# Kernel tuning notes

Hardware: AMD Instinct MI355X
Metric: run time of the kernel (lower is better)

Reference implementation:

```python
import math
import jax, jax.numpy as jnp
import numpy as np

HEAD_DIM = 64
N_HEAD = 8
INIT_SIZE = 1200  # -> 1201 embeddings, origin_shift = 601


def rel_sinusoidal_pos_embed(seq_len, dim=HEAD_DIM):
    """Matches RelativeSinusoidalPositionalEmbedding(dim, padding_idx=0, init_size=1200)."""
    num = INIT_SIZE + 1  # 1201
    half = dim // 2
    inv_freq = jnp.exp(jnp.arange(half, dtype=jnp.float32) * -(math.log(10000.0) / (half - 1)))
    pos = jnp.arange(-(num // 2), num // 2, dtype=jnp.float32)  # -601 .. 599 (1201 values)
    ang = pos[:, None] * inv_freq[None, :]                      # [num, half]
    w = jnp.concatenate([jnp.sin(ang), jnp.cos(ang)], axis=1)   # [num, dim]
    w = w.at[0].set(0.0)  # padding_idx row zeroed
    origin_shift = num // 2 + 1  # 601
    idx = jnp.arange(-seq_len, seq_len) + origin_shift          # [2L]
    return w[idx]                                               # [2L, dim]


def _shift(BD):
    # BD: [b, n, L, 2L] -> [b, n, L, L] (Transformer-XL skew trick)
    b, n, L, _ = BD.shape
    BD = jnp.pad(BD, ((0, 0), (0, 0), (0, 0), (0, 1)))  # [b,n,L,2L+1]
    BD = BD.reshape(b, n, 2 * L + 1, L)[:, :, :-1].reshape(b, n, L, 2 * L)
    return BD[:, :, :, L:]


def _transpose_shift(E):
    # E: [b, n, L, 2L] -> [b, n, L, L]
    b, n, L, _ = E.shape
    E = jnp.pad(E, ((0, 0), (0, 0), (0, 0), (0, 1))).reshape(b, n, 2 * L + 1, L)
    idx = jnp.arange(L) * 2 + 1
    return jnp.swapaxes(E[:, :, idx, :], -1, -2)


def setup_inputs() -> dict:
    key = jax.random.key(0)
    k1, k2, k3, k4 = jax.random.split(key, 4)
    B, L, D = 8, 512, 512
    x = jax.random.normal(k1, (B, L, D), dtype=jnp.float32)
    mask = jnp.ones((B, L), dtype=jnp.int32)
    W_qkv = jax.random.normal(k2, (D, 3 * D), dtype=jnp.float32) * (1.0 / math.sqrt(D))
    r_r_bias = jax.random.normal(k3, (N_HEAD, HEAD_DIM), dtype=jnp.float32) * 0.1
    r_w_bias = jax.random.normal(k4, (N_HEAD, HEAD_DIM), dtype=jnp.float32) * 0.1
    return {"x": x, "mask": mask, "W_qkv": W_qkv, "r_r_bias": r_r_bias, "r_w_bias": r_w_bias}


def reference(x, mask, W_qkv, r_r_bias, r_w_bias):
    B, L, D = x.shape
    scale = math.sqrt(HEAD_DIM)
    pos = rel_sinusoidal_pos_embed(L)  # [2L, head_dim], detached constant

    qkv = x @ W_qkv  # [B, L, 3D]
    q, k, v = jnp.split(qkv, 3, axis=-1)
    q = q.reshape(B, L, N_HEAD, HEAD_DIM).transpose(0, 2, 1, 3)  # [B,H,L,d]
    k = k.reshape(B, L, N_HEAD, HEAD_DIM).transpose(0, 2, 1, 3)
    v = v.reshape(B, L, N_HEAD, HEAD_DIM).transpose(0, 2, 1, 3)

    rw_head_q = q + r_r_bias[None, :, None, :]
    AC = jnp.einsum('bnqd,bnkd->bnqk', rw_head_q, k)              # [B,H,L,L]
    D_ = jnp.einsum('nd,ld->nl', r_w_bias, pos)[None, :, None, :] # [1,H,1,2L]
    B_ = jnp.einsum('bnqd,ld->bnql', q, pos)                      # [B,H,L,2L]
    E_ = jnp.einsum('bnqd,ld->bnql', k, pos)                      # [B,H,L,2L]

    BDE = _shift(B_ + D_) + _transpose_shift(E_)                  # [B,H,L,L]
    attn = (AC + BDE) / scale
    attn = jnp.where(mask[:, None, None, :] == 0, -jnp.inf, attn)
    attn = jax.nn.softmax(attn, axis=-1)

    out = jnp.matmul(attn, v)                                     # [B,H,L,d]
    return out.transpose(0, 2, 1, 3).reshape(B, L, D)
```

## Files before the change

kernel.cpp:

```cpp
#include <hip/hip_runtime.h>
#include <hip/hip_bf16.h>
#include <math.h>

#define LSEQ 512
#define DDIM 192

typedef __attribute__((ext_vector_type(8))) short s16x8;
typedef __attribute__((ext_vector_type(4))) float f32x4;
typedef unsigned short ushort_t;
typedef unsigned int uint_t;

#define MFMA16(a, b, c) __builtin_amdgcn_mfma_f32_16x16x32_bf16(a, b, c, 0, 0, 0)

__device__ __forceinline__ ushort_t f2b(float f) {
  union { float f; uint_t u; } v; v.f = f;
  uint_t r = (v.u + 0x7FFFu + ((v.u >> 16) & 1u)) >> 16;
  return (ushort_t)r;
}
__device__ __forceinline__ float b2f(ushort_t u) {
  union { uint_t u; float f; } v; v.u = ((uint_t)u) << 16;
  return v.f;
}

typedef const __attribute__((address_space(1))) void g_void_t;
typedef __attribute__((address_space(3))) void lds_void_t;
__device__ __forceinline__ void load_lds16(const void* g, void* l) {
  __builtin_amdgcn_global_load_lds((g_void_t*)g, (lds_void_t*)l, 16, 0, 0);
}

__device__ __forceinline__ size_t kswz(size_t row, int d) {
  return row * DDIM + (size_t)((d & 0x1C7) | ((((d >> 3) & 7) ^ ((int)row & 7)) << 3));
}

__global__ void cast_x(const float* __restrict__ x, ushort_t* __restrict__ xb) {
  const int i = (blockIdx.x * 256 + threadIdx.x) * 8;
  const int row = i >> 9, k = i & 511;
  float4 a = *(const float4*)(x + i);
  float4 b = *(const float4*)(x + i + 4);
  uint4 o;
  o.x = (uint_t)f2b(a.x) | ((uint_t)f2b(a.y) << 16);
  o.y = (uint_t)f2b(a.z) | ((uint_t)f2b(a.w) << 16);
  o.z = (uint_t)f2b(b.x) | ((uint_t)f2b(b.y) << 16);
  o.w = (uint_t)f2b(b.z) | ((uint_t)f2b(b.w) << 16);
  const int dst = row * 512 + (k & 448) + (((((k >> 3) & 7) ^ (row & 7))) << 3);
  *(uint4*)(xb + dst) = o;
}

__global__ void cast_transpose_w(const float* __restrict__ W, ushort_t* __restrict__ Wt) {
  __shared__ float tile[32][33];
  const int tx = threadIdx.x & 31, ty = threadIdx.x >> 5;
  const int k0 = blockIdx.x * 32, n0 = blockIdx.y * 32;
#pragma unroll
  for (int i = 0; i < 4; ++i)
    tile[ty + i * 8][tx] = W[(size_t)(k0 + ty + i * 8) * 1536 + n0 + tx];
  __syncthreads();
#pragma unroll
  for (int i = 0; i < 4; ++i) {
    const int n = n0 + ty + i * 8, k = k0 + tx;
    Wt[(size_t)n * 512 + (k & 448) + ((((k >> 3) & 7) ^ (n & 7)) << 3) + (k & 7)] =
        f2b(tile[tx][ty + i * 8]);
  }
}

__global__ __launch_bounds__(256, 3) void qkv_gemm(
    const ushort_t* __restrict__ xb, const ushort_t* __restrict__ Wt,
    const float* __restrict__ rr,
    ushort_t* __restrict__ Qt, ushort_t* __restrict__ Kt, ushort_t* __restrict__ Vt) {
  __shared__ __align__(16) ushort_t ldsA[2][64 * 64];
  __shared__ __align__(16) ushort_t ldsB[2][128 * 64];
  const int tid = threadIdx.x;
  const int w = tid >> 6, lane = tid & 63, lo = lane & 15, hi = lane >> 4;
  const int wm = w >> 1, wn = w & 1;
  const int id = blockIdx.x;
  const int mp = id & 63, np = id >> 6;
  const int m0 = mp * 64, n0 = np * 128;

  f32x4 acc[2][4];
  const f32x4 zero4 = {0.f, 0.f, 0.f, 0.f};
#pragma unroll
  for (int i = 0; i < 2; ++i)
#pragma unroll
    for (int j = 0; j < 4; ++j) acc[i][j] = zero4;

  const char* asrc = (const char*)xb + (size_t)m0 * 1024;
  const char* bsrc = (const char*)Wt + (size_t)n0 * 1024;

#define STAGE_QKV(buf, ks)                                                     \
  {                                                                            \
    char* la = (char*)&ldsA[buf][0] + w * 1024;                                \
    char* lb = (char*)&ldsB[buf][0] + w * 1024;                                \
    _Pragma("unroll") for (int it = 0; it < 2; ++it) {                         \
      const int X = it * 4096 + tid * 16;                                      \
      load_lds16(asrc + (size_t)(X >> 7) * 1024 + (ks) * 128 + (X & 127),      \
                 la + it * 4096);                                              \
    }                                                                          \
    _Pragma("unroll") for (int it = 0; it < 4; ++it) {                         \
      const int X = it * 4096 + tid * 16;                                      \
      load_lds16(bsrc + (size_t)(X >> 7) * 1024 + (ks) * 128 + (X & 127),      \
                 lb + it * 4096);                                              \
    }                                                                          \
  }

  STAGE_QKV(0, 0);
  for (int ks = 0; ks < 8; ++ks) {
    const int cur = ks & 1;
    __syncthreads();
    if (ks < 7) STAGE_QKV(cur ^ 1, ks + 1);
    const char* Ab = (const char*)&ldsA[cur][0];
    const char* Bb = (const char*)&ldsB[cur][0];
#pragma unroll
    for (int kh = 0; kh < 2; ++kh) {
      const int sw = ((kh * 4 + hi) ^ (lo & 7)) << 4;
      s16x8 a[2], bf[4];
#pragma unroll
      for (int i = 0; i < 2; ++i)
        a[i] = *(const s16x8*)(Ab + (wm * 32 + i * 16 + lo) * 128 + sw);
#pragma unroll
      for (int j = 0; j < 4; ++j)
        bf[j] = *(const s16x8*)(Bb + (wn * 64 + j * 16 + lo) * 128 + sw);
#pragma unroll
      for (int i = 0; i < 2; ++i)
#pragma unroll
        for (int j = 0; j < 4; ++j)
          acc[i][j] = MFMA16(a[i], bf[j], acc[i][j]);
    }
  }

  const int sect = n0 >> 9;
  const int h = ((n0 + wn * 64) >> 6) & 7;
  const int mrow0 = m0 + wm * 32;

  if (sect == 0) {
    float bias[4];
#pragma unroll
    for (int j = 0; j < 4; ++j) bias[j] = rr[h * 64 + j * 16 + lo];
#pragma unroll
    for (int i = 0; i < 2; ++i)
#pragma unroll
      for (int r = 0; r < 4; ++r) {
        const int m = mrow0 + i * 16 + hi * 4 + r;
        const size_t row = ((size_t)(m >> 9) * 8 + h) * 512 + (m & 511);
#pragma unroll
        for (int j = 0; j < 4; ++j)
          Qt[row * DDIM + j * 16 + lo] = f2b((acc[i][j][r] + bias[j]) * 0.125f);
      }
  } else if (sect == 1) {
#pragma unroll
    for (int i = 0; i < 2; ++i)
#pragma unroll
      for (int r = 0; r < 4; ++r) {
        const int m = mrow0 + i * 16 + hi * 4 + r;
        const size_t row = ((size_t)(m >> 9) * 8 + h) * 512 + (m & 511);
#pragma unroll
        for (int j = 0; j < 4; ++j)
          Kt[row * DDIM + ((((j * 2 + (lo >> 3)) ^ (m & 7)) << 3) | (lo & 7))] =
              f2b(acc[i][j][r]);
      }
  } else {
#pragma unroll
    for (int i = 0; i < 2; ++i) {
      const int b = (mrow0 + i * 16) >> 9;
      const int l0 = (mrow0 + i * 16 + hi * 4) & 511;
#pragma unroll
      for (int j = 0; j < 4; ++j) {
        ushort4 pk;
        pk.x = f2b(acc[i][j][0]); pk.y = f2b(acc[i][j][1]);
        pk.z = f2b(acc[i][j][2]); pk.w = f2b(acc[i][j][3]);
        *(ushort4*)&Vt[(((size_t)b * 8 + h) * 64 + j * 16 + lo) * 512 + l0] = pk;
      }
    }
  }
}

__global__ void build_feats(ushort_t* __restrict__ Qt, ushort_t* __restrict__ Kt,
                            const float* __restrict__ rr, const float* __restrict__ rw) {
  const int idx = blockIdx.x * blockDim.x + threadIdx.x;
  const int hf = idx & 31;
  const size_t row = (size_t)(idx >> 5);
  const int l = (int)(row & 511);
  const int hh = (int)((row >> 9) & 7);

  const float f = __expf(-(float)hf * 0.29710775393472f);
  float s0, c0, s1, c1;
  __sincosf((float)l * f, &s0, &c0);
  __sincosf((float)(l + 1) * f, &s1, &c1);

  const size_t qb = row * DDIM;
  const float qr_s = b2f(Qt[qb + hf]);
  const float qr_c = b2f(Qt[qb + 32 + hf]);
  const float qw_s = qr_s + 0.125f * (rw[hh * 64 + hf] - rr[hh * 64 + hf]);
  const float qw_c = qr_c + 0.125f * (rw[hh * 64 + 32 + hf] - rr[hh * 64 + 32 + hf]);
  Qt[qb + 64 + hf]  = f2b(qw_s * c0 + qw_c * s0);
  Qt[qb + 96 + hf]  = f2b(qw_c * c0 - qw_s * s0);
  Qt[qb + 128 + hf] = f2b(0.125f * s1);
  Qt[qb + 160 + hf] = f2b(0.125f * c1);

  const float k_s = b2f(Kt[kswz(row, hf)]);
  const float k_c = b2f(Kt[kswz(row, 32 + hf)]);
  Kt[kswz(row, 64 + hf)]  = f2b(s1);
  Kt[kswz(row, 96 + hf)]  = f2b(c1);
  Kt[kswz(row, 128 + hf)] = f2b(k_s * c0 + k_c * s0);
  Kt[kswz(row, 160 + hf)] = f2b(k_c * c0 - k_s * s0);
}

__global__ __launch_bounds__(256, 2) void attn_kernel(
    const ushort_t* __restrict__ Qt, const ushort_t* __restrict__ Kt,
    const ushort_t* __restrict__ Vt, const int* __restrict__ mask,
    float* __restrict__ out) {
  __shared__ __align__(16) ushort_t ldsK[2][64 * DDIM];
  __shared__ __align__(16) ushort_t P[4][16][72];

  const int tid = threadIdx.x;
  const int w = tid >> 6;
  const int lane = tid & 63, lo = lane & 15, hi = lane >> 4;
  const int id = blockIdx.x;
  const int bh = id & 63, qg = id >> 6;
  const int b = bh >> 3, h = bh & 7;
  const int q0 = qg * 64 + w * 16;
  const size_t qrow0 = (size_t)bh * LSEQ + q0;

  s16x8 qf[6];
#pragma unroll
  for (int ks = 0; ks < 6; ++ks)
    qf[ks] = *(const s16x8*)(Qt + (qrow0 + lo) * DDIM + ks * 32 + hi * 8);

  const f32x4 zero4 = {0.f, 0.f, 0.f, 0.f};
  f32x4 o[4];
#pragma unroll
  for (int j = 0; j < 4; ++j) o[j] = zero4;
  float mrun = -3.0e38f, lrun = 0.f;

  const char* ksrc = (const char*)(Kt + (size_t)bh * LSEQ * DDIM);
  const ushort_t* vbase = Vt + ((size_t)bh * 64 + lo) * 512 + hi * 8;

  {
    char* d = (char*)&ldsK[0][0] + w * 1024;
#pragma unroll
    for (int it = 0; it < 6; ++it)
      load_lds16(ksrc + it * 4096 + tid * 16, d + it * 4096);
  }

  for (int kt = 0; kt < 8; ++kt) {
    const int cur = kt & 1;
    __syncthreads();
    if (kt < 7) {
      const char* s = ksrc + (kt + 1) * 24576;
      char* d = (char*)&ldsK[cur ^ 1][0] + w * 1024;
#pragma unroll
      for (int it = 0; it < 6; ++it)
        load_lds16(s + it * 4096 + tid * 16, d + it * 4096);
    }

    f32x4 sf[4];
#pragma unroll
    for (int f = 0; f < 4; ++f) sf[f] = zero4;
    const char* kl = (const char*)&ldsK[cur][0];
    __builtin_amdgcn_s_setprio(1);
#pragma unroll
    for (int ks = 0; ks < 6; ++ks) {
      const int swb = ((ks * 4 + hi) ^ (lo & 7)) << 4;
#pragma unroll
      for (int f = 0; f < 4; ++f) {
        s16x8 ka = *(const s16x8*)(kl + (f * 16 + lo) * 384 + swb);
        sf[f] = MFMA16(ka, qf[ks], sf[f]);
      }
    }
    __builtin_amdgcn_s_setprio(0);

    const int mk = mask[b * LSEQ + kt * 64 + lane];
    if (__ballot(mk == 0) != 0ull) {
#pragma unroll
      for (int f = 0; f < 4; ++f)
#pragma unroll
        for (int r = 0; r < 4; ++r)
          if (__shfl(mk, f * 16 + hi * 4 + r) == 0) sf[f][r] = -3.0e38f;
    }

    float tm = fmaxf(fmaxf(sf[0][0], sf[0][1]), fmaxf(sf[0][2], sf[0][3]));
#pragma unroll
    for (int f = 1; f < 4; ++f)
      tm = fmaxf(tm, fmaxf(fmaxf(sf[f][0], sf[f][1]), fmaxf(sf[f][2], sf[f][3])));
    tm = fmaxf(tm, __shfl_xor(tm, 16));
    tm = fmaxf(tm, __shfl_xor(tm, 32));

    if (!__all(tm - mrun <= 8.0f)) {
      const float mnew = fmaxf(mrun, tm);
      const float corr = __expf(mrun - mnew);
      lrun *= corr;
      mrun = mnew;
      float cq[4];
#pragma unroll
      for (int r = 0; r < 4; ++r) cq[r] = __shfl(corr, hi * 4 + r);
#pragma unroll
      for (int j = 0; j < 4; ++j)
#pragma unroll
        for (int r = 0; r < 4; ++r) o[j][r] *= cq[r];
    }

    float ts = 0.f;
#pragma unroll
    for (int f = 0; f < 4; ++f)
#pragma unroll
      for (int r = 0; r < 4; ++r) {
        sf[f][r] = __expf(sf[f][r] - mrun);
        ts += sf[f][r];
      }
    ts += __shfl_xor(ts, 16);
    ts += __shfl_xor(ts, 32);
    lrun += ts;

#pragma unroll
    for (int f = 0; f < 4; ++f) {
      __hip_bfloat162 p0 = __float22bfloat162_rn(make_float2(sf[f][0], sf[f][1]));
      __hip_bfloat162 p1 = __float22bfloat162_rn(make_float2(sf[f][2], sf[f][3]));
      uint2 u;
      __builtin_memcpy(&u.x, &p0, 4);
      __builtin_memcpy(&u.y, &p1, 4);
      *(uint2*)&P[w][lo][f * 16 + hi * 4] = u;
    }

    __builtin_amdgcn_s_setprio(1);
#pragma unroll
    for (int kh = 0; kh < 2; ++kh) {
      s16x8 pa = *(const s16x8*)&P[w][lo][kh * 32 + hi * 8];
#pragma unroll
      for (int j = 0; j < 4; ++j) {
        s16x8 vb = *(const s16x8*)(vbase + (size_t)j * 16 * 512 + kt * 64 + kh * 32);
        o[j] = MFMA16(pa, vb, o[j]);
      }
    }
    __builtin_amdgcn_s_setprio(0);
  }

  float lq[4];
#pragma unroll
  for (int r = 0; r < 4; ++r) lq[r] = 1.0f / __shfl(lrun, hi * 4 + r);
#pragma unroll
  for (int j = 0; j < 4; ++j)
#pragma unroll
    for (int r = 0; r < 4; ++r)
      out[((size_t)b * LSEQ + q0 + hi * 4 + r) * 512 + h * 64 + j * 16 + lo] =
          o[j][r] * lq[r];
}

extern "C" void kernel_launch(void* const* d_in, const int* in_sizes, int n_in,
                              void* d_out, int out_size, void* d_ws, size_t ws_size,
                              hipStream_t stream) {
  const float* x    = (const float*)d_in[0];
  const int*   mask = (const int*)d_in[1];
  const float* W    = (const float*)d_in[2];
  const float* rr   = (const float*)d_in[3];
  const float* rw   = (const float*)d_in[4];
  float* out = (float*)d_out;

  char* ws = (char*)d_ws;
  ushort_t* xb = (ushort_t*)(ws);
  ushort_t* Wt = (ushort_t*)(ws + 4194304);
  ushort_t* Qt = (ushort_t*)(ws + 5767168);
  ushort_t* Kt = (ushort_t*)(ws + 18350080);
  ushort_t* Vt = (ushort_t*)(ws + 30932992);

  cast_x<<<1024, 256, 0, stream>>>(x, xb);
  cast_transpose_w<<<dim3(16, 48), 256, 0, stream>>>(W, Wt);
  qkv_gemm<<<768, 256, 0, stream>>>(xb, Wt, rr, Qt, Kt, Vt);
  build_feats<<<4096, 256, 0, stream>>>(Qt, Kt, rr, rw);
  attn_kernel<<<512, 256, 0, stream>>>(Qt, Kt, Vt, mask, out);
}
```

Measured before the change: 60.75 us.

## Process 32 query rows per wave in attention and merge cast kernels

The attention kernel now uses 2 waves of 128 threads per block, each handling 32 query rows as two 16-row MFMA tiles. Each K fragment read from LDS and each V fragment loaded from global memory then feeds two MFMAs, which halves the fragment traffic per row. The two input-cast kernels are also merged into one launch to cut a kernel launch. In exchange, register pressure rises and there are fewer waves per block (launch bounds 128,1), which may reduce latency hiding and occupancy.

```diff
diff --git a/kernel.cpp b/kernel.cpp
--- a/kernel.cpp
+++ b/kernel.cpp
@@ -32,33 +32,36 @@
   return row * DDIM + (size_t)((d & 0x1C7) | ((((d >> 3) & 7) ^ ((int)row & 7)) << 3));
 }
 
-__global__ void cast_x(const float* __restrict__ x, ushort_t* __restrict__ xb) {
-  const int i = (blockIdx.x * 256 + threadIdx.x) * 8;
-  const int row = i >> 9, k = i & 511;
-  float4 a = *(const float4*)(x + i);
-  float4 b = *(const float4*)(x + i + 4);
-  uint4 o;
-  o.x = (uint_t)f2b(a.x) | ((uint_t)f2b(a.y) << 16);
-  o.y = (uint_t)f2b(a.z) | ((uint_t)f2b(a.w) << 16);
-  o.z = (uint_t)f2b(b.x) | ((uint_t)f2b(b.y) << 16);
-  o.w = (uint_t)f2b(b.z) | ((uint_t)f2b(b.w) << 16);
-  const int dst = row * 512 + (k & 448) + (((((k >> 3) & 7) ^ (row & 7))) << 3);
-  *(uint4*)(xb + dst) = o;
-}
-
-__global__ void cast_transpose_w(const float* __restrict__ W, ushort_t* __restrict__ Wt) {
+__global__ void cast_all(const float* __restrict__ x, const float* __restrict__ W,
+                         ushort_t* __restrict__ xb, ushort_t* __restrict__ Wt) {
   __shared__ float tile[32][33];
-  const int tx = threadIdx.x & 31, ty = threadIdx.x >> 5;
-  const int k0 = blockIdx.x * 32, n0 = blockIdx.y * 32;
-#pragma unroll
-  for (int i = 0; i < 4; ++i)
-    tile[ty + i * 8][tx] = W[(size_t)(k0 + ty + i * 8) * 1536 + n0 + tx];
-  __syncthreads();
-#pragma unroll
-  for (int i = 0; i < 4; ++i) {
-    const int n = n0 + ty + i * 8, k = k0 + tx;
-    Wt[(size_t)n * 512 + (k & 448) + ((((k >> 3) & 7) ^ (n & 7)) << 3) + (k & 7)] =
-        f2b(tile[tx][ty + i * 8]);
+  const int id = blockIdx.x;
+  if (id < 1024) {
+    const int i = (id * 256 + threadIdx.x) * 8;
+    const int row = i >> 9, k = i & 511;
+    float4 a = *(const float4*)(x + i);
+    float4 b = *(const float4*)(x + i + 4);
+    uint4 o;
+    o.x = (uint_t)f2b(a.x) | ((uint_t)f2b(a.y) << 16);
+    o.y = (uint_t)f2b(a.z) | ((uint_t)f2b(a.w) << 16);
+    o.z = (uint_t)f2b(b.x) | ((uint_t)f2b(b.y) << 16);
+    o.w = (uint_t)f2b(b.z) | ((uint_t)f2b(b.w) << 16);
+    const int dst = row * 512 + (k & 448) + (((((k >> 3) & 7) ^ (row & 7))) << 3);
+    *(uint4*)(xb + dst) = o;
+  } else {
+    const int wid = id - 1024;
+    const int tx = threadIdx.x & 31, ty = threadIdx.x >> 5;
+    const int k0 = (wid & 15) * 32, n0 = (wid >> 4) * 32;
+#pragma unroll
+    for (int i = 0; i < 4; ++i)
+      tile[ty + i * 8][tx] = W[(size_t)(k0 + ty + i * 8) * 1536 + n0 + tx];
+    __syncthreads();
+#pragma unroll
+    for (int i = 0; i < 4; ++i) {
+      const int n = n0 + ty + i * 8, k = k0 + tx;
+      Wt[(size_t)n * 512 + (k & 448) + ((((k >> 3) & 7) ^ (n & 7)) << 3) + (k & 7)] =
+          f2b(tile[tx][ty + i * 8]);
+    }
   }
 }
 
@@ -203,12 +206,12 @@
   Kt[kswz(row, 160 + hf)] = f2b(k_c * c0 - k_s * s0);
 }
 
-__global__ __launch_bounds__(256, 2) void attn_kernel(
+__global__ __launch_bounds__(128, 1) void attn_kernel(
     const ushort_t* __restrict__ Qt, const ushort_t* __restrict__ Kt,
     const ushort_t* __restrict__ Vt, const int* __restrict__ mask,
     float* __restrict__ out) {
   __shared__ __align__(16) ushort_t ldsK[2][64 * DDIM];
-  __shared__ __align__(16) ushort_t P[4][16][72];
+  __shared__ __align__(16) ushort_t P[2][32][72];
 
   const int tid = threadIdx.x;
   const int w = tid >> 6;
@@ -216,44 +219,47 @@
   const int id = blockIdx.x;
   const int bh = id & 63, qg = id >> 6;
   const int b = bh >> 3, h = bh & 7;
-  const int q0 = qg * 64 + w * 16;
+  const int q0 = qg * 64 + w * 32;
   const size_t qrow0 = (size_t)bh * LSEQ + q0;
 
-  s16x8 qf[6];
-#pragma unroll
-  for (int ks = 0; ks < 6; ++ks)
-    qf[ks] = *(const s16x8*)(Qt + (qrow0 + lo) * DDIM + ks * 32 + hi * 8);
+  s16x8 qf[2][6];
+#pragma unroll
+  for (int i = 0; i < 2; ++i)
+#pragma unroll
+    for (int ks = 0; ks < 6; ++ks)
+      qf[i][ks] = *(const s16x8*)(Qt + (qrow0 + i * 16 + lo) * DDIM + ks * 32 + hi * 8);
 
   const f32x4 zero4 = {0.f, 0.f, 0.f, 0.f};
-  f32x4 o[4];
-#pragma unroll
-  for (int j = 0; j < 4; ++j) o[j] = zero4;
-  float mrun = -3.0e38f, lrun = 0.f;
+  f32x4 o[2][4];
+#pragma unroll
+  for (int i = 0; i < 2; ++i)
+#pragma unroll
+    for (int j = 0; j < 4; ++j) o[i][j] = zero4;
+  float mrun[2] = {-3.0e38f, -3.0e38f}, lrun[2] = {0.f, 0.f};
 
   const char* ksrc = (const char*)(Kt + (size_t)bh * LSEQ * DDIM);
   const ushort_t* vbase = Vt + ((size_t)bh * 64 + lo) * 512 + hi * 8;
 
-  {
-    char* d = (char*)&ldsK[0][0] + w * 1024;
-#pragma unroll
-    for (int it = 0; it < 6; ++it)
-      load_lds16(ksrc + it * 4096 + tid * 16, d + it * 4096);
-  }
+#pragma unroll
+  for (int it = 0; it < 12; ++it)
+    load_lds16(ksrc + it * 2048 + tid * 16, (char*)&ldsK[0][0] + it * 2048 + tid * 16);
 
   for (int kt = 0; kt < 8; ++kt) {
     const int cur = kt & 1;
     __syncthreads();
     if (kt < 7) {
       const char* s = ksrc + (kt + 1) * 24576;
-      char* d = (char*)&ldsK[cur ^ 1][0] + w * 1024;
-#pragma unroll
-      for (int it = 0; it < 6; ++it)
-        load_lds16(s + it * 4096 + tid * 16, d + it * 4096);
-    }
-
-    f32x4 sf[4];
-#pragma unroll
-    for (int f = 0; f < 4; ++f) sf[f] = zero4;
+      char* d = (char*)&ldsK[cur ^ 1][0];
+#pragma unroll
+      for (int it = 0; it < 12; ++it)
+        load_lds16(s + it * 2048 + tid * 16, d + it * 2048 + tid * 16);
+    }
+
+    f32x4 sf[2][4];
+#pragma unroll
+    for (int i = 0; i < 2; ++i)
+#pragma unroll
+      for (int f = 0; f < 4; ++f) sf[i][f] = zero4;
     const char* kl = (const char*)&ldsK[cur][0];
     __builtin_amdgcn_s_setprio(1);
 #pragma unroll
@@ -262,7 +268,8 @@
 #pragma unroll
       for (int f = 0; f < 4; ++f) {
         s16x8 ka = *(const s16x8*)(kl + (f * 16 + lo) * 384 + swb);
-        sf[f] = MFMA16(ka, qf[ks], sf[f]);
+        sf[0][f] = MFMA16(ka, qf[0][ks], sf[0][f]);
+        sf[1][f] = MFMA16(ka, qf[1][ks], sf[1][f]);
       }
     }
     __builtin_amdgcn_s_setprio(0);
@@ -273,74 +280,86 @@
       for (int f = 0; f < 4; ++f)
 #pragma unroll
         for (int r = 0; r < 4; ++r)
-          if (__shfl(mk, f * 16 + hi * 4 + r) == 0) sf[f][r] = -3.0e38f;
-    }
-
-    float tm = fmaxf(fmaxf(sf[0][0], sf[0][1]), fmaxf(sf[0][2], sf[0][3]));
-#pragma unroll
-    for (int f = 1; f < 4; ++f)
-      tm = fmaxf(tm, fmaxf(fmaxf(sf[f][0], sf[f][1]), fmaxf(sf[f][2], sf[f][3])));
-    tm = fmaxf(tm, __shfl_xor(tm, 16));
-    tm = fmaxf(tm, __shfl_xor(tm, 32));
-
-    if (!__all(tm - mrun <= 8.0f)) {
-      const float mnew = fmaxf(mrun, tm);
-      const float corr = __expf(mrun - mnew);
-      lrun *= corr;
-      mrun = mnew;
-      float cq[4];
-#pragma unroll
-      for (int r = 0; r < 4; ++r) cq[r] = __shfl(corr, hi * 4 + r);
-#pragma unroll
-      for (int j = 0; j < 4; ++j)
-#pragma unroll
-        for (int r = 0; r < 4; ++r) o[j][r] *= cq[r];
-    }
-
-    float ts = 0.f;
-#pragma unroll
-    for (int f = 0; f < 4; ++f)
-#pragma unroll
-      for (int r = 0; r < 4; ++r) {
-        sf[f][r] = __expf(sf[f][r] - mrun);
-        ts += sf[f][r];
-      }
-    ts += __shfl_xor(ts, 16);
-    ts += __shfl_xor(ts, 32);
-    lrun += ts;
-
-#pragma unroll
-    for (int f = 0; f < 4; ++f) {
-      __hip_bfloat162 p0 = __float22bfloat162_rn(make_float2(sf[f][0], sf[f][1]));
-      __hip_bfloat162 p1 = __float22bfloat162_rn(make_float2(sf[f][2], sf[f][3]));
-      uint2 u;
-      __builtin_memcpy(&u.x, &p0, 4);
-      __builtin_memcpy(&u.y, &p1, 4);
-      *(uint2*)&P[w][lo][f * 16 + hi * 4] = u;
+          if (__shfl(mk, f * 16 + hi * 4 + r) == 0) {
+            sf[0][f][r] = -3.0e38f;
+            sf[1][f][r] = -3.0e38f;
+          }
+    }
+
+#pragma unroll
+    for (int i = 0; i < 2; ++i) {
+      float tm = fmaxf(fmaxf(sf[i][0][0], sf[i][0][1]), fmaxf(sf[i][0][2], sf[i][0][3]));
+#pragma unroll
+      for (int f = 1; f < 4; ++f)
+        tm = fmaxf(tm, fmaxf(fmaxf(sf[i][f][0], sf[i][f][1]),
+                             fmaxf(sf[i][f][2], sf[i][f][3])));
+      tm = fmaxf(tm, __shfl_xor(tm, 16));
+      tm = fmaxf(tm, __shfl_xor(tm, 32));
+
+      if (!__all(tm - mrun[i] <= 8.0f)) {
+        const float mnew = fmaxf(mrun[i], tm);
+        const float corr = __expf(mrun[i] - mnew);
+        lrun[i] *= corr;
+        mrun[i] = mnew;
+        float cq[4];
+#pragma unroll
+        for (int r = 0; r < 4; ++r) cq[r] = __shfl(corr, hi * 4 + r);
+#pragma unroll
+        for (int j = 0; j < 4; ++j)
+#pragma unroll
+          for (int r = 0; r < 4; ++r) o[i][j][r] *= cq[r];
+      }
+
+      float ts = 0.f;
+#pragma unroll
+      for (int f = 0; f < 4; ++f)
+#pragma unroll
+        for (int r = 0; r < 4; ++r) {
+          sf[i][f][r] = __expf(sf[i][f][r] - mrun[i]);
+          ts += sf[i][f][r];
+        }
+      ts += __shfl_xor(ts, 16);
+      ts += __shfl_xor(ts, 32);
+      lrun[i] += ts;
+
+#pragma unroll
+      for (int f = 0; f < 4; ++f) {
+        __hip_bfloat162 p0 = __float22bfloat162_rn(make_float2(sf[i][f][0], sf[i][f][1]));
+        __hip_bfloat162 p1 = __float22bfloat162_rn(make_float2(sf[i][f][2], sf[i][f][3]));
+        uint2 u;
+        __builtin_memcpy(&u.x, &p0, 4);
+        __builtin_memcpy(&u.y, &p1, 4);
+        *(uint2*)&P[w][i * 16 + lo][f * 16 + hi * 4] = u;
+      }
     }
 
     __builtin_amdgcn_s_setprio(1);
 #pragma unroll
     for (int kh = 0; kh < 2; ++kh) {
-      s16x8 pa = *(const s16x8*)&P[w][lo][kh * 32 + hi * 8];
+      s16x8 pa0 = *(const s16x8*)&P[w][lo][kh * 32 + hi * 8];
+      s16x8 pa1 = *(const s16x8*)&P[w][16 + lo][kh * 32 + hi * 8];
 #pragma unroll
       for (int j = 0; j < 4; ++j) {
         s16x8 vb = *(const s16x8*)(vbase + (size_t)j * 16 * 512 + kt * 64 + kh * 32);
-        o[j] = MFMA16(pa, vb, o[j]);
+        o[0][j] = MFMA16(pa0, vb, o[0][j]);
+        o[1][j] = MFMA16(pa1, vb, o[1][j]);
       }
     }
     __builtin_amdgcn_s_setprio(0);
   }
 
-  float lq[4];
-#pragma unroll
-  for (int r = 0; r < 4; ++r) lq[r] = 1.0f / __shfl(lrun, hi * 4 + r);
-#pragma unroll
-  for (int j = 0; j < 4; ++j)
-#pragma unroll
-    for (int r = 0; r < 4; ++r)
-      out[((size_t)b * LSEQ + q0 + hi * 4 + r) * 512 + h * 64 + j * 16 + lo] =
-          o[j][r] * lq[r];
+#pragma unroll
+  for (int i = 0; i < 2; ++i) {
+    float lq[4];
+#pragma unroll
+    for (int r = 0; r < 4; ++r) lq[r] = 1.0f / __shfl(lrun[i], hi * 4 + r);
+#pragma unroll
+    for (int j = 0; j < 4; ++j)
+#pragma unroll
+      for (int r = 0; r < 4; ++r)
+        out[((size_t)b * LSEQ + q0 + i * 16 + hi * 4 + r) * 512 + h * 64 + j * 16 + lo] =
+            o[i][j][r] * lq[r];
+  }
 }
 
 extern "C" void kernel_launch(void* const* d_in, const int* in_sizes, int n_in,
@@ -360,9 +379,8 @@
   ushort_t* Kt = (ushort_t*)(ws + 18350080);
   ushort_t* Vt = (ushort_t*)(ws + 30932992);
 
-  cast_x<<<1024, 256, 0, stream>>>(x, xb);
-  cast_transpose_w<<<dim3(16, 48), 256, 0, stream>>>(W, Wt);
+  cast_all<<<1792, 256, 0, stream>>>(x, W, xb, Wt);
   qkv_gemm<<<768, 256, 0, stream>>>(xb, Wt, rr, Qt, Kt, Vt);
   build_feats<<<4096, 256, 0, stream>>>(Qt, Kt, rr, rw);
-  attn_kernel<<<512, 256, 0, stream>>>(Qt, Kt, Vt, mask, out);
-}
+  attn_kernel<<<512, 128, 0, stream>>>(Qt, Kt, Vt, mask, out);
+}
```

New measurement: 60.87 us. Within noise of the previous version (+0.2%).
